# Optimization experiments

Measured on AMD Instinct MI355X. Metric: run time of the kernel, lower is better.

## Reference

```python
import jax, jax.numpy as jnp
import numpy as np

MARGIN = 0.3  # init kwarg, mode='norm'


def _pairwise_dist(X):
    # squared euclidean distances, then safe sqrt (matches euc_dist(X.t()).sqrt())
    sq = jnp.sum(X * X, axis=1)                      # [n]
    d2 = sq[:, None] + sq[None, :] - 2.0 * (X @ X.T)  # [n, n]
    d2 = jnp.maximum(d2, 0.0)
    # safe sqrt: avoid inf derivative at 0 (diagonal); forward value identical
    return jnp.where(d2 > 0.0, jnp.sqrt(jnp.where(d2 > 0.0, d2, 1.0)), 0.0)


def setup_inputs() -> dict:
    key = jax.random.key(0)
    kx, ky = jax.random.split(key)
    X = jax.random.normal(kx, (4096, 2048), dtype=jnp.float32)
    Y = jax.random.randint(ky, (4096,), 0, 128, dtype=jnp.int64)
    return {"X": X, "Y": Y}


def reference(X, Y):
    dist = _pairwise_dist(X)                         # [n, n]
    mask = Y[:, None] == Y[None, :]                  # same-identity mask [n, n]
    inf = jnp.array(jnp.inf, dtype=dist.dtype)
    # hardest positive per anchor: max over same-label entries
    dist_ap = jnp.max(jnp.where(mask, dist, -inf), axis=1)  # [n]
    # hardest negative per anchor: min over different-label entries
    dist_an = jnp.min(jnp.where(mask, inf, dist), axis=1)   # [n]
    # mode == 'norm': mean hinge
    return jnp.mean(jnp.maximum(dist_ap - dist_an + MARGIN, 0.0))
```

## Files before the change

kernel.cpp:

```cpp
#include <hip/hip_runtime.h>
#include <hip/hip_bf16.h>
#include <hip/hip_fp8.h>

typedef __attribute__((ext_vector_type(2))) float f32x2;
typedef __attribute__((ext_vector_type(4))) int i32x4;
typedef __attribute__((ext_vector_type(8))) int i32x8;
typedef __attribute__((ext_vector_type(16))) float f32x16;

#define MARGIN 0.3f
#define BIGF 3.0e38f

#if defined(__has_builtin)
#if __has_builtin(__builtin_amdgcn_cvt_pk_fp8_f32) && \
    __has_builtin(__builtin_amdgcn_cvt_pk_f32_fp8)
#define HAVE_PK_FP8 1
#endif
#endif

__device__ __forceinline__ void gl2lds16(const void* g, void* l) {
    __builtin_amdgcn_global_load_lds(
        (const __attribute__((address_space(1))) void*)g,
        (__attribute__((address_space(3))) void*)l,
        16, 0, 0);
}

__global__ __launch_bounds__(256) void convert_norm_kernel(
    const float* __restrict__ X, unsigned char* __restrict__ Xq,
    float* __restrict__ nrm, unsigned* __restrict__ ap,
    unsigned* __restrict__ an, unsigned* __restrict__ cnt, int K) {
    const int wave = threadIdx.x >> 6, lane = threadIdx.x & 63;
    const int row = blockIdx.x * 4 + wave;
    const float* xr = X + (size_t)row * K;
    unsigned char* xqr = Xq + (size_t)row * K;
    float s = 0.0f;
    for (int c = lane * 8; c < K; c += 64 * 8) {
        float4 v0 = *(const float4*)(xr + c);
        float4 v1 = *(const float4*)(xr + c + 4);
#if defined(HAVE_PK_FP8)
        int w0 = 0, w1 = 0;
        w0 = __builtin_amdgcn_cvt_pk_fp8_f32(v0.x, v0.y, w0, false);
        w0 = __builtin_amdgcn_cvt_pk_fp8_f32(v0.z, v0.w, w0, true);
        w1 = __builtin_amdgcn_cvt_pk_fp8_f32(v1.x, v1.y, w1, false);
        w1 = __builtin_amdgcn_cvt_pk_fp8_f32(v1.z, v1.w, w1, true);
        f32x2 d0 = __builtin_amdgcn_cvt_pk_f32_fp8(w0, false);
        f32x2 d1 = __builtin_amdgcn_cvt_pk_f32_fp8(w0, true);
        f32x2 d2 = __builtin_amdgcn_cvt_pk_f32_fp8(w1, false);
        f32x2 d3 = __builtin_amdgcn_cvt_pk_f32_fp8(w1, true);
        s += d0[0]*d0[0] + d0[1]*d0[1] + d1[0]*d1[0] + d1[1]*d1[1];
        s += d2[0]*d2[0] + d2[1]*d2[1] + d3[0]*d3[0] + d3[1]*d3[1];
        uint2 u; u.x = (unsigned)w0; u.y = (unsigned)w1;
        *(uint2*)(xqr + c) = u;
#else
        float f[8] = {v0.x, v0.y, v0.z, v0.w, v1.x, v1.y, v1.z, v1.w};
        union { unsigned char b[8]; uint2 u; } p;
#pragma unroll
        for (int i = 0; i < 8; i++) {
            __hip_fp8_e4m3 q(f[i]);
            p.b[i] = q.__x;
            float d = (float)q;
            s += d * d;
        }
        *(uint2*)(xqr + c) = p.u;
#endif
    }
    for (int off = 32; off > 0; off >>= 1) s += __shfl_xor(s, off, 64);
    if (lane == 0) {
        nrm[row] = s;
        ap[row] = 0u;
        an[row] = 0x7F800000u;
        if (row == 0) *cnt = 0u;
    }
}

__global__ __launch_bounds__(256, 4) void gemm_reduce_kernel(
    const unsigned char* __restrict__ Xq, const float* __restrict__ nrm,
    const int* __restrict__ Y, unsigned* __restrict__ ap,
    unsigned* __restrict__ an, unsigned* __restrict__ cnt,
    float* __restrict__ out, int N, int K) {
    __shared__ __align__(16) unsigned char sA[128 * 128];
    __shared__ __align__(16) unsigned char sB[128 * 128];
    __shared__ int sYr[128], sYc[128];
    __shared__ float sNr[128], sNc[128];
    __shared__ float redmax[4][64], redmin[4][64];
    __shared__ float credmax[2][2][64], credmin[2][2][64];
    __shared__ float lsum[4];
    __shared__ unsigned s_done;

    const int tid = threadIdx.x;
    const int wave = tid >> 6;
    const int lane = tid & 63;
    const int m = lane & 31;
    const int h = lane >> 5;
    const int wr = wave >> 1;
    const int wc = wave & 1;

    int j = 0;
    {
        const int b = blockIdx.x;
        while ((j + 1) * (j + 2) / 2 <= b) j++;
    }
    const int r = blockIdx.x - j * (j + 1) / 2;
    const int rowBase = r * 128;
    const int colBase = j * 128;

    if (tid < 128) {
        sYr[tid] = Y[rowBase + tid];
        sNr[tid] = nrm[rowBase + tid];
    } else {
        int t = tid - 128;
        sYc[t] = Y[colBase + t];
        sNc[t] = nrm[colBase + t];
    }

    f32x16 acc[2][2];
#pragma unroll
    for (int si = 0; si < 2; si++)
#pragma unroll
        for (int sj = 0; sj < 2; sj++)
#pragma unroll
            for (int rr = 0; rr < 16; rr++) acc[si][sj][rr] = 0.0f;

    const int rsub = lane >> 3;
    const int jchunk = (lane & 7) ^ rsub;
    const unsigned char* gA = Xq + (size_t)(rowBase + wave * 32 + rsub) * K + jchunk * 16;
    const unsigned char* gB = Xq + (size_t)(colBase + wave * 32 + rsub) * K + jchunk * 16;
    unsigned char* lA = sA + wave * 4096;
    unsigned char* lB = sB + wave * 4096;
    const size_t g8 = (size_t)8 * K;

    const int e = m & 7;
    const int nit = K >> 7;

    for (int it = 0; it < nit; it++) {
        const size_t go = (size_t)it * 128;
#pragma unroll
        for (int g = 0; g < 4; g++) {
            gl2lds16(gA + go + g * g8, lA + g * 1024);
            gl2lds16(gB + go + g * g8, lB + g * 1024);
        }
        __syncthreads();

#pragma unroll
        for (int s = 0; s < 2; s++) {
            const int c0 = s * 4 + h * 2;
            i32x8 af[2], bf[2];
#pragma unroll
            for (int si = 0; si < 2; si++) {
                const unsigned char* base = sA + (wr * 64 + si * 32 + m) * 128;
                i32x4 lo = *(const i32x4*)(base + ((c0 ^ e) * 16));
                i32x4 hi = *(const i32x4*)(base + (((c0 + 1) ^ e) * 16));
                af[si] = __builtin_shufflevector(lo, hi, 0, 1, 2, 3, 4, 5, 6, 7);
            }
#pragma unroll
            for (int sj = 0; sj < 2; sj++) {
                const unsigned char* base = sB + (wc * 64 + sj * 32 + m) * 128;
                i32x4 lo = *(const i32x4*)(base + ((c0 ^ e) * 16));
                i32x4 hi = *(const i32x4*)(base + (((c0 + 1) ^ e) * 16));
                bf[sj] = __builtin_shufflevector(lo, hi, 0, 1, 2, 3, 4, 5, 6, 7);
            }
#pragma unroll
            for (int si = 0; si < 2; si++)
#pragma unroll
                for (int sj = 0; sj < 2; sj++)
                    acc[si][sj] = __builtin_amdgcn_mfma_scale_f32_32x32x64_f8f6f4(
                        af[si], bf[sj], acc[si][sj], 0 ,
                        0 , 0, 127 ,
                        0, 127 );
        }
        __syncthreads();
    }

    float cmx0 = -1.0f, cmx1 = -1.0f, cmn0 = BIGF, cmn1 = BIGF;

#pragma unroll
    for (int si = 0; si < 2; si++)
#pragma unroll
        for (int reg = 0; reg < 16; reg++) {
            const int row64 = si * 32 + (reg & 3) + 8 * (reg >> 2) + 4 * h;
            const int rIdx = wr * 64 + row64;
            const int yr = sYr[rIdx];
            const float nr = sNr[rIdx];
            float dp = -1.0f, dn = BIGF;
            {
                const int cIdx = wc * 64 + m;
                float d2 = nr + sNc[cIdx] - 2.0f * acc[si][0][reg];
                float d = sqrtf(fmaxf(d2, 0.0f));
                bool same = (yr == sYc[cIdx]);
                float p = same ? d : -1.0f;
                float n = same ? BIGF : d;
                dp = fmaxf(dp, p); dn = fminf(dn, n);
                cmx0 = fmaxf(cmx0, p); cmn0 = fminf(cmn0, n);
            }
            {
                const int cIdx = wc * 64 + 32 + m;
                float d2 = nr + sNc[cIdx] - 2.0f * acc[si][1][reg];
                float d = sqrtf(fmaxf(d2, 0.0f));
                bool same = (yr == sYc[cIdx]);
                float p = same ? d : -1.0f;
                float n = same ? BIGF : d;
                dp = fmaxf(dp, p); dn = fminf(dn, n);
                cmx1 = fmaxf(cmx1, p); cmn1 = fminf(cmn1, n);
            }
            for (int off = 1; off < 32; off <<= 1) {
                dp = fmaxf(dp, __shfl_xor(dp, off, 64));
                dn = fminf(dn, __shfl_xor(dn, off, 64));
            }
            if (m == 0) {
                redmax[wave][row64] = dp;
                redmin[wave][row64] = dn;
            }
        }

    {
        float mx = fmaxf(cmx0, __shfl_xor(cmx0, 32, 64));
        float mn = fminf(cmn0, __shfl_xor(cmn0, 32, 64));
        if (h == 0) { credmax[wr][wc][m] = mx; credmin[wr][wc][m] = mn; }
        mx = fmaxf(cmx1, __shfl_xor(cmx1, 32, 64));
        mn = fminf(cmn1, __shfl_xor(cmn1, 32, 64));
        if (h == 0) { credmax[wr][wc][32 + m] = mx; credmin[wr][wc][32 + m] = mn; }
    }
    __syncthreads();

    if (tid < 128) {
        const int g2 = tid >> 6, i64 = tid & 63;
        float mx = fmaxf(redmax[g2 * 2][i64], redmax[g2 * 2 + 1][i64]);
        float mn = fminf(redmin[g2 * 2][i64], redmin[g2 * 2 + 1][i64]);
        atomicMax(&ap[rowBase + tid], __float_as_uint(fmaxf(mx, 0.0f)));
        atomicMin(&an[rowBase + tid], __float_as_uint(mn));
        float cx = fmaxf(credmax[0][g2][i64], credmax[1][g2][i64]);
        float cn = fminf(credmin[0][g2][i64], credmin[1][g2][i64]);
        atomicMax(&ap[colBase + tid], __float_as_uint(fmaxf(cx, 0.0f)));
        atomicMin(&an[colBase + tid], __float_as_uint(cn));
    }

    __syncthreads();
    if (tid == 0) {
        __threadfence();
        s_done = atomicAdd(cnt, 1u);
    }
    __syncthreads();
    if (s_done == gridDim.x - 1) {
        __threadfence();
        float s = 0.0f;
        for (int i = tid; i < N; i += 256) {
            unsigned ua = __hip_atomic_load(&ap[i], __ATOMIC_RELAXED,
                                            __HIP_MEMORY_SCOPE_AGENT);
            unsigned ub = __hip_atomic_load(&an[i], __ATOMIC_RELAXED,
                                            __HIP_MEMORY_SCOPE_AGENT);
            s += fmaxf(__uint_as_float(ua) - __uint_as_float(ub) + MARGIN, 0.0f);
        }
        for (int off = 32; off > 0; off >>= 1) s += __shfl_xor(s, off, 64);
        if (lane == 0) lsum[wave] = s;
        __syncthreads();
        if (tid == 0)
            out[0] = (lsum[0] + lsum[1] + lsum[2] + lsum[3]) / (float)N;
    }
}

extern "C" void kernel_launch(void* const* d_in, const int* in_sizes, int n_in,
                              void* d_out, int out_size, void* d_ws, size_t ws_size,
                              hipStream_t stream) {
    const float* X = (const float*)d_in[0];
    const int* Y = (const int*)d_in[1];
    float* out = (float*)d_out;
    const int N = in_sizes[1];
    const int K = in_sizes[0] / N;

    char* ws = (char*)d_ws;
    unsigned char* Xq = (unsigned char*)ws;
    float* nrm = (float*)(ws + (size_t)N * K);
    unsigned* ap = (unsigned*)((char*)nrm + (size_t)N * 4);
    unsigned* an = (unsigned*)((char*)ap + (size_t)N * 4);
    unsigned* cnt = (unsigned*)((char*)an + (size_t)N * 4);

    convert_norm_kernel<<<N / 4, 256, 0, stream>>>(X, Xq, nrm, ap, an, cnt, K);
    const int NB = N / 128;
    const int nblocks = NB * (NB + 1) / 2;
    gemm_reduce_kernel<<<nblocks, 256, 0, stream>>>(Xq, nrm, Y, ap, an, cnt,
                                                    out, N, K);
}
```

Before: 133.4 us.

## Split K across two blocks per tile with global atomic partial sums

Each output tile is now computed by two blocks, each handling half of the K dimension. They accumulate partial dot products into a zeroed global buffer with float atomics, and the last-arriving block computes distances and row/column hinge reductions. This aims to fill more compute units, at the cost of a large memset, heavy global atomic traffic and a serialized epilogue.

```diff
diff --git a/kernel.cpp b/kernel.cpp
--- a/kernel.cpp
+++ b/kernel.cpp
@@ -27,7 +27,7 @@
 __global__ __launch_bounds__(256) void convert_norm_kernel(
     const float* __restrict__ X, unsigned char* __restrict__ Xq,
     float* __restrict__ nrm, unsigned* __restrict__ ap,
-    unsigned* __restrict__ an, unsigned* __restrict__ cnt, int K) {
+    unsigned* __restrict__ an, int K) {
     const int wave = threadIdx.x >> 6, lane = threadIdx.x & 63;
     const int row = blockIdx.x * 4 + wave;
     const float* xr = X + (size_t)row * K;
@@ -68,7 +68,6 @@
         nrm[row] = s;
         ap[row] = 0u;
         an[row] = 0x7F800000u;
-        if (row == 0) *cnt = 0u;
     }
 }
 
@@ -76,15 +75,14 @@
     const unsigned char* __restrict__ Xq, const float* __restrict__ nrm,
     const int* __restrict__ Y, unsigned* __restrict__ ap,
     unsigned* __restrict__ an, unsigned* __restrict__ cnt,
+    unsigned* __restrict__ tilecnt, float* __restrict__ gbuf,
     float* __restrict__ out, int N, int K) {
     __shared__ __align__(16) unsigned char sA[128 * 128];
     __shared__ __align__(16) unsigned char sB[128 * 128];
     __shared__ int sYr[128], sYc[128];
     __shared__ float sNr[128], sNc[128];
-    __shared__ float redmax[4][64], redmin[4][64];
-    __shared__ float credmax[2][2][64], credmin[2][2][64];
     __shared__ float lsum[4];
-    __shared__ unsigned s_done;
+    __shared__ unsigned s_done, s_t;
 
     const int tid = threadIdx.x;
     const int wave = tid >> 6;
@@ -94,12 +92,14 @@
     const int wr = wave >> 1;
     const int wc = wave & 1;
 
+    const int t = blockIdx.x >> 1;
+    const int khalf = blockIdx.x & 1;
+
     int j = 0;
     {
-        const int b = blockIdx.x;
-        while ((j + 1) * (j + 2) / 2 <= b) j++;
-    }
-    const int r = blockIdx.x - j * (j + 1) / 2;
+        while ((j + 1) * (j + 2) / 2 <= t) j++;
+    }
+    const int r = t - j * (j + 1) / 2;
     const int rowBase = r * 128;
     const int colBase = j * 128;
 
@@ -107,9 +107,9 @@
         sYr[tid] = Y[rowBase + tid];
         sNr[tid] = nrm[rowBase + tid];
     } else {
-        int t = tid - 128;
-        sYc[t] = Y[colBase + t];
-        sNc[t] = nrm[colBase + t];
+        int tt = tid - 128;
+        sYc[tt] = Y[colBase + tt];
+        sNc[tt] = nrm[colBase + tt];
     }
 
     f32x16 acc[2][2];
@@ -130,8 +130,10 @@
 
     const int e = m & 7;
     const int nit = K >> 7;
-
-    for (int it = 0; it < nit; it++) {
+    const int it0 = khalf * (nit / 2);
+    const int it1 = it0 + nit / 2;
+
+    for (int it = it0; it < it1; it++) {
         const size_t go = (size_t)it * 128;
 #pragma unroll
         for (int g = 0; g < 4; g++) {
@@ -170,67 +172,71 @@
         __syncthreads();
     }
 
-    float cmx0 = -1.0f, cmx1 = -1.0f, cmn0 = BIGF, cmn1 = BIGF;
-
+    float* gt = gbuf + (size_t)t * 16384;
 #pragma unroll
     for (int si = 0; si < 2; si++)
 #pragma unroll
-        for (int reg = 0; reg < 16; reg++) {
-            const int row64 = si * 32 + (reg & 3) + 8 * (reg >> 2) + 4 * h;
-            const int rIdx = wr * 64 + row64;
-            const int yr = sYr[rIdx];
-            const float nr = sNr[rIdx];
-            float dp = -1.0f, dn = BIGF;
-            {
-                const int cIdx = wc * 64 + m;
-                float d2 = nr + sNc[cIdx] - 2.0f * acc[si][0][reg];
-                float d = sqrtf(fmaxf(d2, 0.0f));
-                bool same = (yr == sYc[cIdx]);
-                float p = same ? d : -1.0f;
-                float n = same ? BIGF : d;
-                dp = fmaxf(dp, p); dn = fminf(dn, n);
-                cmx0 = fmaxf(cmx0, p); cmn0 = fminf(cmn0, n);
-            }
-            {
-                const int cIdx = wc * 64 + 32 + m;
-                float d2 = nr + sNc[cIdx] - 2.0f * acc[si][1][reg];
-                float d = sqrtf(fmaxf(d2, 0.0f));
-                bool same = (yr == sYc[cIdx]);
-                float p = same ? d : -1.0f;
-                float n = same ? BIGF : d;
-                dp = fmaxf(dp, p); dn = fminf(dn, n);
-                cmx1 = fmaxf(cmx1, p); cmn1 = fminf(cmn1, n);
-            }
-            for (int off = 1; off < 32; off <<= 1) {
-                dp = fmaxf(dp, __shfl_xor(dp, off, 64));
-                dn = fminf(dn, __shfl_xor(dn, off, 64));
-            }
-            if (m == 0) {
-                redmax[wave][row64] = dp;
-                redmin[wave][row64] = dn;
-            }
-        }
-
-    {
-        float mx = fmaxf(cmx0, __shfl_xor(cmx0, 32, 64));
-        float mn = fminf(cmn0, __shfl_xor(cmn0, 32, 64));
-        if (h == 0) { credmax[wr][wc][m] = mx; credmin[wr][wc][m] = mn; }
-        mx = fmaxf(cmx1, __shfl_xor(cmx1, 32, 64));
-        mn = fminf(cmn1, __shfl_xor(cmn1, 32, 64));
-        if (h == 0) { credmax[wr][wc][32 + m] = mx; credmin[wr][wc][32 + m] = mn; }
-    }
-    __syncthreads();
-
-    if (tid < 128) {
-        const int g2 = tid >> 6, i64 = tid & 63;
-        float mx = fmaxf(redmax[g2 * 2][i64], redmax[g2 * 2 + 1][i64]);
-        float mn = fminf(redmin[g2 * 2][i64], redmin[g2 * 2 + 1][i64]);
-        atomicMax(&ap[rowBase + tid], __float_as_uint(fmaxf(mx, 0.0f)));
-        atomicMin(&an[rowBase + tid], __float_as_uint(mn));
-        float cx = fmaxf(credmax[0][g2][i64], credmax[1][g2][i64]);
-        float cn = fminf(credmin[0][g2][i64], credmin[1][g2][i64]);
-        atomicMax(&ap[colBase + tid], __float_as_uint(fmaxf(cx, 0.0f)));
-        atomicMin(&an[colBase + tid], __float_as_uint(cn));
+        for (int sj = 0; sj < 2; sj++)
+#pragma unroll
+            for (int reg = 0; reg < 16; reg++) {
+                const int rIdx = wr * 64 + si * 32 + (reg & 3) + 8 * (reg >> 2) + 4 * h;
+                const int cIdx = wc * 64 + sj * 32 + m;
+                atomicAdd(&gt[rIdx * 128 + cIdx], acc[si][sj][reg]);
+            }
+    __syncthreads();
+
+    if (tid == 0) {
+        __threadfence();
+        s_t = atomicAdd(&tilecnt[t], 1u);
+    }
+    __syncthreads();
+
+    if (s_t == 1) {
+        __threadfence();
+        {
+            const int i2 = tid >> 1, ch = tid & 1;
+            const int yrI = sYr[i2];
+            const float nrI = sNr[i2];
+            float pmx = -1.0f, pmn = BIGF;
+            for (int c2 = 0; c2 < 64; c2++) {
+                const int c = ch * 64 + c2;
+                float g = __hip_atomic_load(&gt[i2 * 128 + c], __ATOMIC_RELAXED,
+                                            __HIP_MEMORY_SCOPE_AGENT);
+                float d2v = nrI + sNc[c] - 2.0f * g;
+                float d = sqrtf(fmaxf(d2v, 0.0f));
+                bool same = (yrI == sYc[c]);
+                pmx = fmaxf(pmx, same ? d : -1.0f);
+                pmn = fminf(pmn, same ? BIGF : d);
+            }
+            pmx = fmaxf(pmx, __shfl_xor(pmx, 1, 64));
+            pmn = fminf(pmn, __shfl_xor(pmn, 1, 64));
+            if (ch == 0) {
+                atomicMax(&ap[rowBase + i2], __float_as_uint(fmaxf(pmx, 0.0f)));
+                atomicMin(&an[rowBase + i2], __float_as_uint(pmn));
+            }
+        }
+        {
+            const int c2 = tid >> 1, rh = tid & 1;
+            const int ycI = sYc[c2];
+            const float ncI = sNc[c2];
+            float pmx = -1.0f, pmn = BIGF;
+            for (int s2 = 0; s2 < 64; s2++) {
+                const int i = rh * 64 + s2;
+                float g = __hip_atomic_load(&gt[i * 128 + c2], __ATOMIC_RELAXED,
+                                            __HIP_MEMORY_SCOPE_AGENT);
+                float d2v = sNr[i] + ncI - 2.0f * g;
+                float d = sqrtf(fmaxf(d2v, 0.0f));
+                bool same = (sYr[i] == ycI);
+                pmx = fmaxf(pmx, same ? d : -1.0f);
+                pmn = fminf(pmn, same ? BIGF : d);
+            }
+            pmx = fmaxf(pmx, __shfl_xor(pmx, 1, 64));
+            pmn = fminf(pmn, __shfl_xor(pmn, 1, 64));
+            if (rh == 0) {
+                atomicMax(&ap[colBase + c2], __float_as_uint(fmaxf(pmx, 0.0f)));
+                atomicMin(&an[colBase + c2], __float_as_uint(pmn));
+            }
+        }
     }
 
     __syncthreads();
@@ -266,16 +272,22 @@
     const int N = in_sizes[1];
     const int K = in_sizes[0] / N;
 
+    const int NB = N / 128;
+    const int ntiles = NB * (NB + 1) / 2;
+
     char* ws = (char*)d_ws;
     unsigned char* Xq = (unsigned char*)ws;
     float* nrm = (float*)(ws + (size_t)N * K);
     unsigned* ap = (unsigned*)((char*)nrm + (size_t)N * 4);
     unsigned* an = (unsigned*)((char*)ap + (size_t)N * 4);
     unsigned* cnt = (unsigned*)((char*)an + (size_t)N * 4);
-
-    convert_norm_kernel<<<N / 4, 256, 0, stream>>>(X, Xq, nrm, ap, an, cnt, K);
-    const int NB = N / 128;
-    const int nblocks = NB * (NB + 1) / 2;
-    gemm_reduce_kernel<<<nblocks, 256, 0, stream>>>(Xq, nrm, Y, ap, an, cnt,
-                                                    out, N, K);
-}
+    unsigned* tilecnt = cnt + 1;
+    float* gbuf = (float*)((char*)tilecnt + (size_t)ntiles * 4);
+
+    const size_t zbytes = 4 + (size_t)ntiles * 4 + (size_t)ntiles * 16384 * 4;
+    hipMemsetAsync(cnt, 0, zbytes, stream);
+
+    convert_norm_kernel<<<N / 4, 256, 0, stream>>>(X, Xq, nrm, ap, an, K);
+    gemm_reduce_kernel<<<ntiles * 2, 256, 0, stream>>>(Xq, nrm, Y, ap, an, cnt,
+                                                       tilecnt, gbuf, out, N, K);
+}
```

Result: slower. 388.4 us (+191.2%).
